# Performance work log

Hardware: AMD Instinct MI355X
Metric: run time of the kernel (lower is better)

The kernel has to match this reference:

```python
import jax, jax.numpy as jnp
import numpy as np

VOXEL_SIZE = 0.05  # from init_kwargs


def _voxel_ds(pts, voxel_size, key, L):
    """Voxel-grid downsample one cloud (N,3): mean of points per occupied voxel,
    then resample L voxel centroids (uniform with replacement among valid voxels).
    Static shapes throughout (jit/vmap friendly)."""
    N = pts.shape[0]
    mn = jnp.min(pts, axis=0)
    v = jnp.floor((pts - mn) / voxel_size).astype(jnp.int32)      # (N,3) voxel coords >= 0
    dims = jnp.max(v, axis=0) + 1                                  # traced grid extents
    lin = (v[:, 0] * dims[1] + v[:, 1]) * dims[2] + v[:, 2]        # linearized voxel id
    order = jnp.argsort(lin)
    sl = lin[order]
    is_new = jnp.concatenate([jnp.ones((1,), bool), sl[1:] != sl[:-1]])
    seg = jnp.cumsum(is_new) - 1                                   # compact segment id per sorted point
    num_vox = seg[-1] + 1                                          # traced count of occupied voxels
    sums = jax.ops.segment_sum(pts[order], seg, num_segments=N)    # (N,3) padded
    cnt = jax.ops.segment_sum(jnp.ones((N,), pts.dtype), seg, num_segments=N)
    means = sums / jnp.maximum(cnt, 1.0)[:, None]                  # voxel centroids
    # random resample L centroids among the first num_vox valid segments
    u = jax.random.uniform(key, (L,))
    idx = jnp.minimum((u * num_vox.astype(u.dtype)).astype(jnp.int32), num_vox - 1)
    return means[idx]                                              # (L,3)


def _voxel_layer(x, voxel_size, L, key):
    # x: (B,3,N) -> (B,3,L)
    B = x.shape[0]
    pts = jnp.transpose(x, (0, 2, 1))                              # (B,N,3)
    keys = jax.random.split(key, B)
    out = jax.vmap(lambda p, k: _voxel_ds(p, voxel_size, k, L))(pts, keys)
    return jnp.transpose(out, (0, 2, 1))                           # (B,3,L)


def setup_inputs() -> dict:
    key = jax.random.key(0)
    x = jax.random.uniform(key, (16, 3, 262144), dtype=jnp.float32)
    return {"x": x}


def reference(x):
    B, _, N = x.shape
    L1, L2 = N // 2, N // 4
    k1, k2 = jax.random.split(jax.random.key(42))
    voxel_x1 = _voxel_layer(x, VOXEL_SIZE, L1, k1)
    voxel_x2 = _voxel_layer(voxel_x1, 2.0 * VOXEL_SIZE, L2, k2)
    return (voxel_x1, voxel_x2)
```

## Files before the change

kernel.cpp:

```cpp
#include <hip/hip_runtime.h>
#include <stdint.h>


typedef unsigned int u32;
typedef unsigned long long u64;

struct KeyArr { uint32_t k0[16]; uint32_t k1[16]; };

__host__ __device__ inline void tf2x32(uint32_t k0, uint32_t k1,
                                       uint32_t c0, uint32_t c1,
                                       uint32_t& o0, uint32_t& o1) {
  const uint32_t ks0 = k0, ks1 = k1, ks2 = k0 ^ k1 ^ 0x1BD11BDAu;
  uint32_t x0 = c0 + ks0, x1 = c1 + ks1;
#define TF_R(r) { x0 += x1; x1 = (x1 << (r)) | (x1 >> (32 - (r))); x1 ^= x0; }
  TF_R(13) TF_R(15) TF_R(26) TF_R(6)
  x0 += ks1; x1 += ks2 + 1u;
  TF_R(17) TF_R(29) TF_R(16) TF_R(24)
  x0 += ks2; x1 += ks0 + 2u;
  TF_R(13) TF_R(15) TF_R(26) TF_R(6)
  x0 += ks0; x1 += ks1 + 3u;
  TF_R(17) TF_R(29) TF_R(16) TF_R(24)
  x0 += ks1; x1 += ks2 + 4u;
  TF_R(13) TF_R(15) TF_R(26) TF_R(6)
  x0 += ks2; x1 += ks0 + 5u;
#undef TF_R
  o0 = x0; o1 = x1;
}

__global__ void init_kernel(u64* cellsA, u64* cellsB, int ncells) {
  int i = blockIdx.x * blockDim.x + threadIdx.x;
  int stride = gridDim.x * blockDim.x;
  for (int j = i; j < ncells; j += stride) { cellsA[j] = 0ull; cellsB[j] = 0ull; }
}

__global__ void min_kernel(const float* __restrict__ in, int n4,
                           float* __restrict__ pmin) {
  int row = blockIdx.y;
  int PB = gridDim.x;
  const float4* p = (const float4*)in + (size_t)row * n4;
  int base = blockIdx.x * 2048 + threadIdx.x;
  float4 v0 = p[base];
  float4 v1 = p[base + 256];
  float4 v2 = p[base + 512];
  float4 v3 = p[base + 768];
  float4 v4 = p[base + 1024];
  float4 v5 = p[base + 1280];
  float4 v6 = p[base + 1536];
  float4 v7 = p[base + 1792];
  float m0 = fminf(fminf(v0.x, v0.y), fminf(v0.z, v0.w));
  float m1 = fminf(fminf(v1.x, v1.y), fminf(v1.z, v1.w));
  float m2 = fminf(fminf(v2.x, v2.y), fminf(v2.z, v2.w));
  float m3 = fminf(fminf(v3.x, v3.y), fminf(v3.z, v3.w));
  float m4 = fminf(fminf(v4.x, v4.y), fminf(v4.z, v4.w));
  float m5 = fminf(fminf(v5.x, v5.y), fminf(v5.z, v5.w));
  float m6 = fminf(fminf(v6.x, v6.y), fminf(v6.z, v6.w));
  float m7 = fminf(fminf(v7.x, v7.y), fminf(v7.z, v7.w));
  float m = fminf(fminf(fminf(m0, m1), fminf(m2, m3)),
                  fminf(fminf(m4, m5), fminf(m6, m7)));
  for (int off = 32; off > 0; off >>= 1)
    m = fminf(m, __shfl_down(m, off, 64));
  __shared__ float wmin[4];
  int wid = threadIdx.x >> 6;
  if ((threadIdx.x & 63) == 0) wmin[wid] = m;
  __syncthreads();
  if (threadIdx.x == 0)
    pmin[row * PB + blockIdx.x] =
        fminf(fminf(wmin[0], wmin[1]), fminf(wmin[2], wmin[3]));
}

template <int G, int S, bool ATOMIC>
__global__ __launch_bounds__(1024) void accum_kernel(
    const float* __restrict__ in, int N, float vox,
    const float* __restrict__ pmin, int PB, u64* __restrict__ Ap,
    u64* __restrict__ Bp) {
  extern __shared__ u64 lds[];
  u64* lA = lds;
  u64* lB = lds + G;
  int tid = threadIdx.x, b = blockIdx.y;
  for (int i = tid; i < G; i += 1024) { lA[i] = 0ull; lB[i] = 0ull; }

  float m0 = __int_as_float(0x7F800000), m1 = m0, m2 = m0;
  for (int j = 0; j < PB; ++j) {
    m0 = fminf(m0, pmin[(b * 3 + 0) * PB + j]);
    m1 = fminf(m1, pmin[(b * 3 + 1) * PB + j]);
    m2 = fminf(m2, pmin[(b * 3 + 2) * PB + j]);
  }
  __syncthreads();

  int ppb = N / gridDim.x;
  const float* base = in + (size_t)b * 3 * N;
  int start = blockIdx.x * ppb;
  const float4* r0 = (const float4*)(base + start);
  const float4* r1 = (const float4*)(base + N + start);
  const float4* r2 = (const float4*)(base + 2 * N + start);
  int q4 = ppb >> 2;
  for (int i = tid; i < q4; i += 1024) {
    float4 X = r0[i], Y = r1[i], Z = r2[i];
#define PT(px, py, pz) { \
    int v0 = (int)floorf(((px) - m0) / vox); \
    int v1 = (int)floorf(((py) - m1) / vox); \
    int v2 = (int)floorf(((pz) - m2) / vox); \
    int lin = (v0 * S + v1) * S + v2; \
    u32 qx = (u32)((px) * 1048576.0f); \
    u32 qy = (u32)((py) * 1048576.0f); \
    u32 qz = (u32)((pz) * 1048576.0f); \
    atomicAdd(&lA[lin], ((u64)qy << 32) | (u64)qx); \
    atomicAdd(&lB[lin], (1ull << 32) | (u64)qz); }
    PT(X.x, Y.x, Z.x) PT(X.y, Y.y, Z.y) PT(X.z, Y.z, Z.z) PT(X.w, Y.w, Z.w)
#undef PT
  }
  __syncthreads();

  int p = ATOMIC ? 0 : blockIdx.x;
  u64* gA = Ap + ((size_t)p * 16 + b) * G;
  u64* gB = Bp + ((size_t)p * 16 + b) * G;
  for (int c = tid; c < G; c += 1024) {
    if (ATOMIC) {
      u64 Bv = lB[c];
      if (Bv) { atomicAdd(&gA[c], lA[c]); atomicAdd(&gB[c], Bv); }
    } else {
      gA[c] = lA[c];
      gB[c] = lB[c];
    }
  }
}

__global__ void reduce_kernel(int G, int P, const u64* __restrict__ Ap,
                              const u64* __restrict__ Bp,
                              float4* __restrict__ vox4,
                              u32* __restrict__ bcnt) {
  int blk = blockIdx.x, b = blockIdx.y, tid = threadIdx.x;
  int cell = blk * 256 + tid;
  u64 A = 0ull, Bv = 0ull;
  if (cell < G) {
    for (int p = 0; p < P; ++p) {
      size_t o = ((size_t)p * 16 + b) * G + cell;
      A += Ap[o];
      Bv += Bp[o];
    }
  }
  u32 cnt = (u32)(Bv >> 32);
  if (cell < G) {
    float4 o4 = make_float4(0.f, 0.f, 0.f, 0.f);
    if (cnt) {
      double inv = 1.0 / (1048576.0 * (double)cnt);
      o4.x = (float)((double)(u32)A * inv);
      o4.y = (float)((double)(u32)(A >> 32) * inv);
      o4.z = (float)((double)(u32)Bv * inv);
      o4.w = (float)cnt;
    }
    vox4[(size_t)b * G + cell] = o4;
  }
  u64 mask = __ballot(cnt > 0u);
  __shared__ u32 wtot[4];
  if ((tid & 63) == 0) wtot[tid >> 6] = (u32)__popcll(mask);
  __syncthreads();
  if (tid == 0)
    bcnt[b * gridDim.x + blk] = wtot[0] + wtot[1] + wtot[2] + wtot[3];
}

__global__ void compact_b_kernel(int G, const float4* __restrict__ vox4,
                                 const u32* __restrict__ bcnt,
                                 float4* __restrict__ means4,
                                 u32* __restrict__ numvox) {
  int blk = blockIdx.x, nb = gridDim.x, b = blockIdx.y, tid = threadIdx.x;
  int lane = tid & 63, wid = tid >> 6;
  int cell = blk * 256 + tid;
  float4 v = make_float4(0.f, 0.f, 0.f, 0.f);
  bool occ = false;
  if (cell < G) {
    v = vox4[(size_t)b * G + cell];
    occ = v.w > 0.f;
  }
  u64 mask = __ballot(occ);
  u32 prefix = (u32)__popcll(mask & ((1ull << lane) - 1ull));
  __shared__ u32 wb[4];
  if (lane == 0) wb[wid] = (u32)__popcll(mask);
  __syncthreads();
  if (tid == 0) {
    u32 base = 0;
    for (int j = 0; j < blk; ++j) base += bcnt[b * nb + j];
    u32 s = base;
    for (int w = 0; w < 4; ++w) { u32 t = wb[w]; wb[w] = s; s += t; }
    if (blk == nb - 1) numvox[b] = s;
  }
  __syncthreads();
  if (occ) means4[(size_t)b * G + wb[wid] + prefix] = v;
}

__global__ __launch_bounds__(1024) void compact_kernel(
    int G, const u64* __restrict__ Ac, const u64* __restrict__ Bc,
    float4* __restrict__ means4, u32* __restrict__ numvox) {
  int b = blockIdx.x, tid = threadIdx.x, wid = tid >> 6, lane = tid & 63;
  __shared__ u32 wtot[16], wbase[16];
  __shared__ u32 gbase;
  if (tid == 0) gbase = 0u;
  __syncthreads();
  for (int t0 = 0; t0 < G; t0 += 1024) {
    int cell = t0 + tid;
    float4 v = make_float4(0.f, 0.f, 0.f, 0.f);
    u32 cnt = 0u;
    if (cell < G) {
      u64 A = Ac[(size_t)b * G + cell], Bv = Bc[(size_t)b * G + cell];
      cnt = (u32)(Bv >> 32);
      if (cnt) {
        double inv = 1.0 / (1048576.0 * (double)cnt);
        v.x = (float)((double)(u32)A * inv);
        v.y = (float)((double)(u32)(A >> 32) * inv);
        v.z = (float)((double)(u32)Bv * inv);
      }
    }
    bool occ = cnt > 0u;
    u64 mask = __ballot(occ);
    u32 prefix = (u32)__popcll(mask & ((1ull << lane) - 1ull));
    if (lane == 0) wtot[wid] = (u32)__popcll(mask);
    __syncthreads();
    if (tid == 0) {
      u32 s = gbase;
      for (int w = 0; w < 16; ++w) { wbase[w] = s; s += wtot[w]; }
      gbase = s;
    }
    __syncthreads();
    if (occ) means4[(size_t)b * G + wbase[wid] + prefix] = v;
    __syncthreads();
  }
  if (tid == 0) numvox[b] = gbase;
}

__global__ void sample_kernel(int L, int G, const float4* __restrict__ means4,
                              const u32* __restrict__ numvox, KeyArr keys,
                              float* __restrict__ out) {
  int t = blockIdx.x * 256 + threadIdx.x;
  int b = blockIdx.y;
  int l0 = t * 4;
  u32 nv = numvox[b];
  float fnv = (float)nv;
  int nvm1 = (int)nv - 1;
  uint32_t K0 = keys.k0[b], K1 = keys.k1[b];
  float4 m[4];
#pragma unroll
  for (int j = 0; j < 4; ++j) {
    uint32_t w0, w1;
    tf2x32(K0, K1, 0u, (uint32_t)(l0 + j), w0, w1);
    uint32_t bits = w0 ^ w1;
    float u = __uint_as_float((bits >> 9) | 0x3F800000u) - 1.0f;
    int idx = (int)(u * fnv);
    if (idx > nvm1) idx = nvm1;
    m[j] = means4[(size_t)b * G + idx];
  }
  *(float4*)(out + ((size_t)b * 3 + 0) * L + l0) =
      make_float4(m[0].x, m[1].x, m[2].x, m[3].x);
  *(float4*)(out + ((size_t)b * 3 + 1) * L + l0) =
      make_float4(m[0].y, m[1].y, m[2].y, m[3].y);
  *(float4*)(out + ((size_t)b * 3 + 2) * L + l0) =
      make_float4(m[0].z, m[1].z, m[2].z, m[3].z);
}

extern "C" void kernel_launch(void* const* d_in, const int* in_sizes, int n_in,
                              void* d_out, int out_size, void* d_ws,
                              size_t ws_size, hipStream_t stream) {
  const float* x = (const float*)d_in[0];
  float* out = (float*)d_out;

  uint32_t k1a, k1b, k2a, k2b;
  tf2x32(0u, 42u, 0u, 0u, k1a, k1b);
  tf2x32(0u, 42u, 0u, 1u, k2a, k2b);
  KeyArr keys1, keys2;
  for (int b = 0; b < 16; ++b) {
    tf2x32(k1a, k1b, 0u, (uint32_t)b, keys1.k0[b], keys1.k1[b]);
    tf2x32(k2a, k2b, 0u, (uint32_t)b, keys2.k0[b], keys2.k1[b]);
  }

  const int N1 = 262144, L1 = 131072, L2 = 65536, G1 = 8000, G2 = 1000;
  const int PB1 = 32, PB2 = 16, NB1 = 32, NB2 = 4;
  const size_t slice1 = (size_t)16 * G1, slice2 = (size_t)16 * G2;

  const size_t tailBytes = (48 * PB1 + 48 * PB2 + 16 * NB1 + 32) * 4 + 256;
  const size_t bigNeed =
      2ull * 16 * slice1 * 8 + 2ull * slice1 * 16 + tailBytes;
  bool big = ws_size >= bigNeed;

  uint8_t* w = (uint8_t*)d_ws;
  u64 *Ap, *Bp;
  float4 *vox4 = nullptr, *means4;
  uint8_t* tail;
  if (big) {
    Ap = (u64*)w;
    Bp = Ap + 16 * slice1;
    vox4 = (float4*)(Bp + 16 * slice1);
    means4 = vox4 + slice1;
    tail = (uint8_t*)(means4 + slice1);
  } else {
    Ap = (u64*)w;
    Bp = Ap + (slice1 + slice2);
    means4 = (float4*)(Bp + (slice1 + slice2));
    tail = (uint8_t*)(means4 + slice1);
  }
  float* pmin1 = (float*)tail;
  float* pmin2 = pmin1 + 48 * PB1;
  u32* bcnt = (u32*)(pmin2 + 48 * PB2);
  u32* numvox = bcnt + 16 * NB1;

  if (!big) {
    init_kernel<<<dim3(64), dim3(256), 0, stream>>>(
        Ap, Bp, (int)(slice1 + slice2));
  }

  min_kernel<<<dim3(PB1, 48), dim3(256), 0, stream>>>(x, N1 / 4, pmin1);
  if (big) {
    accum_kernel<G1, 20, false>
        <<<dim3(16, 16), dim3(1024), 2 * G1 * 8, stream>>>(x, N1, 0.05f,
                                                           pmin1, PB1, Ap, Bp);
    reduce_kernel<<<dim3(NB1, 16), dim3(256), 0, stream>>>(G1, 16, Ap, Bp,
                                                           vox4, bcnt);
    compact_b_kernel<<<dim3(NB1, 16), dim3(256), 0, stream>>>(
        G1, vox4, bcnt, means4, numvox);
  } else {
    accum_kernel<G1, 20, true>
        <<<dim3(8, 16), dim3(1024), 2 * G1 * 8, stream>>>(x, N1, 0.05f, pmin1,
                                                          PB1, Ap, Bp);
    compact_kernel<<<dim3(16), dim3(1024), 0, stream>>>(G1, Ap, Bp, means4,
                                                        numvox);
  }
  sample_kernel<<<dim3(L1 / 1024, 16), dim3(256), 0, stream>>>(
      L1, G1, means4, numvox, keys1, out);

  float* out2 = out + (size_t)48 * L1;
  min_kernel<<<dim3(PB2, 48), dim3(256), 0, stream>>>(out, L1 / 4, pmin2);
  if (big) {
    accum_kernel<G2, 10, false>
        <<<dim3(16, 16), dim3(1024), 2 * G2 * 8, stream>>>(
            out, L1, 0.1f, pmin2, PB2, Ap, Bp);
    reduce_kernel<<<dim3(NB2, 16), dim3(256), 0, stream>>>(G2, 16, Ap, Bp,
                                                           vox4, bcnt);
    compact_b_kernel<<<dim3(NB2, 16), dim3(256), 0, stream>>>(
        G2, vox4, bcnt, means4, numvox + 16);
  } else {
    accum_kernel<G2, 10, true>
        <<<dim3(8, 16), dim3(1024), 2 * G2 * 8, stream>>>(
            out, L1, 0.1f, pmin2, PB2, Ap + slice1, Bp + slice1);
    compact_kernel<<<dim3(16), dim3(1024), 0, stream>>>(
        G2, Ap + slice1, Bp + slice1, means4, numvox + 16);
  }
  sample_kernel<<<dim3(L2 / 1024, 16), dim3(256), 0, stream>>>(
      L2, G2, means4, numvox + 16, keys2, out2);
}
```

Baseline: 84.29 us.

## Fuse stage-2 min into sampler and merge reduce/compact into one kernel

The first sample kernel now also computes per-block per-axis minima of the points it writes, so the separate stage-2 min kernel over the output can be dropped. The stage-2 reduce and compact kernels are replaced with one 1024-thread kernel per batch that sums the 16 partial accumulators and compacts the occupied cells. The accum kernel's partial-min merge is now a parallel warp reduction instead of a serial loop in every thread. Together these remove two launches and one pass over the intermediate output. The cost is that the sampler does extra reduction work and accum_kernel reads 128 partial minima instead of 16.

```diff
diff --git a/kernel.cpp b/kernel.cpp
--- a/kernel.cpp
+++ b/kernel.cpp
@@ -76,16 +76,21 @@
   extern __shared__ u64 lds[];
   u64* lA = lds;
   u64* lB = lds + G;
+  __shared__ float s_m[3];
   int tid = threadIdx.x, b = blockIdx.y;
   for (int i = tid; i < G; i += 1024) { lA[i] = 0ull; lB[i] = 0ull; }
 
-  float m0 = __int_as_float(0x7F800000), m1 = m0, m2 = m0;
-  for (int j = 0; j < PB; ++j) {
-    m0 = fminf(m0, pmin[(b * 3 + 0) * PB + j]);
-    m1 = fminf(m1, pmin[(b * 3 + 1) * PB + j]);
-    m2 = fminf(m2, pmin[(b * 3 + 2) * PB + j]);
-  }
-  __syncthreads();
+  int wid = tid >> 6, lane = tid & 63;
+  if (wid < 3) {
+    float v = __int_as_float(0x7F800000);
+    for (int j = lane; j < PB; j += 64)
+      v = fminf(v, pmin[(b * 3 + wid) * PB + j]);
+    for (int off = 32; off > 0; off >>= 1)
+      v = fminf(v, __shfl_down(v, off, 64));
+    if (lane == 0) s_m[wid] = v;
+  }
+  __syncthreads();
+  float m0 = s_m[0], m1 = s_m[1], m2 = s_m[2];
 
   int ppb = N / gridDim.x;
   const float* base = in + (size_t)b * 3 * N;
@@ -188,6 +193,42 @@
   if (occ) means4[(size_t)b * G + wb[wid] + prefix] = v;
 }
 
+template <int G>
+__global__ __launch_bounds__(1024) void redcomp_kernel(
+    int P, const u64* __restrict__ Ap, const u64* __restrict__ Bp,
+    float4* __restrict__ means4, u32* __restrict__ numvox) {
+  int b = blockIdx.x, tid = threadIdx.x, wid = tid >> 6, lane = tid & 63;
+  u64 A = 0ull, Bv = 0ull;
+  if (tid < G) {
+    for (int p = 0; p < P; ++p) {
+      size_t o = ((size_t)p * 16 + b) * G + tid;
+      A += Ap[o];
+      Bv += Bp[o];
+    }
+  }
+  u32 cnt = (u32)(Bv >> 32);
+  float4 v = make_float4(0.f, 0.f, 0.f, 0.f);
+  if (cnt) {
+    double inv = 1.0 / (1048576.0 * (double)cnt);
+    v.x = (float)((double)(u32)A * inv);
+    v.y = (float)((double)(u32)(A >> 32) * inv);
+    v.z = (float)((double)(u32)Bv * inv);
+  }
+  bool occ = cnt > 0u;
+  u64 mask = __ballot(occ);
+  u32 prefix = (u32)__popcll(mask & ((1ull << lane) - 1ull));
+  __shared__ u32 wtot[16], wbase[16];
+  if (lane == 0) wtot[wid] = (u32)__popcll(mask);
+  __syncthreads();
+  if (tid == 0) {
+    u32 s = 0;
+    for (int w = 0; w < 16; ++w) { wbase[w] = s; s += wtot[w]; }
+    numvox[b] = s;
+  }
+  __syncthreads();
+  if (occ) means4[(size_t)b * G + wbase[wid] + prefix] = v;
+}
+
 __global__ __launch_bounds__(1024) void compact_kernel(
     int G, const u64* __restrict__ Ac, const u64* __restrict__ Bc,
     float4* __restrict__ means4, u32* __restrict__ numvox) {
@@ -227,9 +268,11 @@
   if (tid == 0) numvox[b] = gbase;
 }
 
+template <bool DOMIN>
 __global__ void sample_kernel(int L, int G, const float4* __restrict__ means4,
                               const u32* __restrict__ numvox, KeyArr keys,
-                              float* __restrict__ out) {
+                              float* __restrict__ out,
+                              float* __restrict__ pmin) {
   int t = blockIdx.x * 256 + threadIdx.x;
   int b = blockIdx.y;
   int l0 = t * 4;
@@ -254,6 +297,31 @@
       make_float4(m[0].y, m[1].y, m[2].y, m[3].y);
   *(float4*)(out + ((size_t)b * 3 + 2) * L + l0) =
       make_float4(m[0].z, m[1].z, m[2].z, m[3].z);
+  if (DOMIN) {
+    float ax = fminf(fminf(m[0].x, m[1].x), fminf(m[2].x, m[3].x));
+    float ay = fminf(fminf(m[0].y, m[1].y), fminf(m[2].y, m[3].y));
+    float az = fminf(fminf(m[0].z, m[1].z), fminf(m[2].z, m[3].z));
+    for (int off = 32; off > 0; off >>= 1) {
+      ax = fminf(ax, __shfl_down(ax, off, 64));
+      ay = fminf(ay, __shfl_down(ay, off, 64));
+      az = fminf(az, __shfl_down(az, off, 64));
+    }
+    __shared__ float wm[4][3];
+    int wid = threadIdx.x >> 6;
+    if ((threadIdx.x & 63) == 0) {
+      wm[wid][0] = ax; wm[wid][1] = ay; wm[wid][2] = az;
+    }
+    __syncthreads();
+    if (threadIdx.x == 0) {
+      int PB = gridDim.x;
+      pmin[(b * 3 + 0) * PB + blockIdx.x] =
+          fminf(fminf(wm[0][0], wm[1][0]), fminf(wm[2][0], wm[3][0]));
+      pmin[(b * 3 + 1) * PB + blockIdx.x] =
+          fminf(fminf(wm[0][1], wm[1][1]), fminf(wm[2][1], wm[3][1]));
+      pmin[(b * 3 + 2) * PB + blockIdx.x] =
+          fminf(fminf(wm[0][2], wm[1][2]), fminf(wm[2][2], wm[3][2]));
+    }
+  }
 }
 
 extern "C" void kernel_launch(void* const* d_in, const int* in_sizes, int n_in,
@@ -272,10 +340,11 @@
   }
 
   const int N1 = 262144, L1 = 131072, L2 = 65536, G1 = 8000, G2 = 1000;
-  const int PB1 = 32, PB2 = 16, NB1 = 32, NB2 = 4;
+  const int PB1 = 32, PB2 = 128, NB1 = 32;
   const size_t slice1 = (size_t)16 * G1, slice2 = (size_t)16 * G2;
 
-  const size_t tailBytes = (48 * PB1 + 48 * PB2 + 16 * NB1 + 32) * 4 + 256;
+  const size_t tailBytes =
+      (48 * PB1 + 48 * PB2 + 16 * NB1 + 32) * 4 + 256;
   const size_t bigNeed =
       2ull * 16 * slice1 * 8 + 2ull * slice1 * 16 + tailBytes;
   bool big = ws_size >= bigNeed;
@@ -322,19 +391,16 @@
     compact_kernel<<<dim3(16), dim3(1024), 0, stream>>>(G1, Ap, Bp, means4,
                                                         numvox);
   }
-  sample_kernel<<<dim3(L1 / 1024, 16), dim3(256), 0, stream>>>(
-      L1, G1, means4, numvox, keys1, out);
+  sample_kernel<true><<<dim3(L1 / 1024, 16), dim3(256), 0, stream>>>(
+      L1, G1, means4, numvox, keys1, out, pmin2);
 
   float* out2 = out + (size_t)48 * L1;
-  min_kernel<<<dim3(PB2, 48), dim3(256), 0, stream>>>(out, L1 / 4, pmin2);
   if (big) {
     accum_kernel<G2, 10, false>
         <<<dim3(16, 16), dim3(1024), 2 * G2 * 8, stream>>>(
             out, L1, 0.1f, pmin2, PB2, Ap, Bp);
-    reduce_kernel<<<dim3(NB2, 16), dim3(256), 0, stream>>>(G2, 16, Ap, Bp,
-                                                           vox4, bcnt);
-    compact_b_kernel<<<dim3(NB2, 16), dim3(256), 0, stream>>>(
-        G2, vox4, bcnt, means4, numvox + 16);
+    redcomp_kernel<G2><<<dim3(16), dim3(1024), 0, stream>>>(
+        16, Ap, Bp, means4, numvox + 16);
   } else {
     accum_kernel<G2, 10, true>
         <<<dim3(8, 16), dim3(1024), 2 * G2 * 8, stream>>>(
@@ -342,6 +408,6 @@
     compact_kernel<<<dim3(16), dim3(1024), 0, stream>>>(
         G2, Ap + slice1, Bp + slice1, means4, numvox + 16);
   }
-  sample_kernel<<<dim3(L2 / 1024, 16), dim3(256), 0, stream>>>(
-      L2, G2, means4, numvox + 16, keys2, out2);
-}
+  sample_kernel<false><<<dim3(L2 / 1024, 16), dim3(256), 0, stream>>>(
+      L2, G2, means4, numvox + 16, keys2, out2, nullptr);
+}
```

Result: faster. 71.92 us (-14.7%).
